# Kernel optimization log

Measured on AMD Instinct MI355X. Metric: run time of the kernel, lower is better.

## Reference

```python
import jax, jax.numpy as jnp
import numpy as np

B = 512          # graphs
M = 200          # nodes per graph
N = B * M        # 102400 total nodes
E = N * 32       # 3,276,800 edges
DIM_IN = 128
K = 30           # SortPool k
F = 32 + 32 + 32 + 1  # concat feature dim = 97


def setup_inputs() -> dict:
    key = jax.random.key(0)
    ks = jax.random.split(key, 20)
    x = jax.random.normal(ks[0], (N, DIM_IN), jnp.float32)
    # within-graph random edges so that batched SortPool is meaningful
    eg = jnp.repeat(jnp.arange(B, dtype=jnp.int32), E // B)  # graph id per edge
    src = eg * M + jax.random.randint(ks[1], (E,), 0, M, dtype=jnp.int32)
    dst = eg * M + jax.random.randint(ks[2], (E,), 0, M, dtype=jnp.int32)
    edge_index = jnp.stack([src, dst])  # [2, E]
    batch = jnp.arange(N, dtype=jnp.int32) // M  # sorted graph assignment

    def lin(k, fi, fo):
        s = 1.0 / np.sqrt(fi)
        return jax.random.uniform(k, (fi, fo), jnp.float32, -s, s)

    inp = {
        "x": x, "edge_index": edge_index, "batch": batch,
        "W1": lin(ks[3], DIM_IN, 32), "b1": jnp.zeros((32,), jnp.float32),
        "W2": lin(ks[4], 32, 32), "b2": jnp.zeros((32,), jnp.float32),
        "W3": lin(ks[5], 32, 32), "b3": jnp.zeros((32,), jnp.float32),
        "W4": lin(ks[6], 32, 1),  "b4": jnp.zeros((1,), jnp.float32),
        "convW1": jax.random.normal(ks[7], (16, 1, 97), jnp.float32) * 0.05,
        "convb1": jnp.zeros((16,), jnp.float32),
        "convW2": jax.random.normal(ks[8], (32, 16, 5), jnp.float32) * 0.05,
        "convb2": jnp.zeros((32,), jnp.float32),
        "linW1": lin(ks[9], 352, 128), "linb1": jnp.zeros((128,), jnp.float32),
        "linW2": lin(ks[10], 128, 1),  "linb2": jnp.zeros((1,), jnp.float32),
    }
    return inp


def _gcn(x, W, b, src, dst, dinv):
    """PyG GCNConv: D^-1/2 (A+I) D^-1/2 X W + b (degrees include self-loops)."""
    xw = x @ W                                   # [N, Fout]
    norm = dinv[src] * dinv[dst]                 # [E]
    agg = jax.ops.segment_sum(xw[src] * norm[:, None], dst, num_segments=N)
    agg = agg + xw * (dinv * dinv)[:, None]      # self-loop term
    return agg + b


def reference(x, edge_index, batch, W1, b1, W2, b2, W3, b3, W4, b4,
              convW1, convb1, convW2, convb2, linW1, linb1, linW2, linb2):
    src, dst = edge_index[0], edge_index[1]
    deg = jax.ops.segment_sum(jnp.ones((E,), x.dtype), dst, num_segments=N) + 1.0
    dinv = jax.lax.rsqrt(deg)

    h1 = jnp.tanh(_gcn(x, W1, b1, src, dst, dinv))
    h2 = jnp.tanh(_gcn(h1, W2, b2, src, dst, dinv))
    h3 = jnp.tanh(_gcn(h2, W3, b3, src, dst, dinv))
    h4 = jnp.tanh(_gcn(h3, W4, b4, src, dst, dinv))
    h = jnp.concatenate([h1, h2, h3, h4], axis=-1)  # [N, 97]

    # SortPool: batch is block-contiguous with M nodes/graph -> dense [B, M, F]
    hd = h.reshape(B, M, F)
    order = jnp.argsort(-hd[:, :, -1], axis=1)[:, :K]          # top-K by last channel
    top = jnp.take_along_axis(hd, order[:, :, None], axis=1)   # [B, K, 97]

    seq = top.reshape(B, 1, K * F)                             # [B, 1, 2910]
    dn = ("NCH", "OIH", "NCH")
    c1 = jax.lax.conv_general_dilated(seq, convW1, (97,), "VALID",
                                      dimension_numbers=dn) + convb1[None, :, None]
    c1 = jax.nn.relu(c1)                                       # [B, 16, 30]
    c1 = c1.reshape(B, 16, 15, 2).max(axis=-1)                 # MaxPool1d(2,2)
    c2 = jax.lax.conv_general_dilated(c1, convW2, (1,), "VALID",
                                      dimension_numbers=dn) + convb2[None, :, None]
    c2 = jax.nn.relu(c2)                                       # [B, 32, 11]

    flat = c2.reshape(B, 352)
    hlin = jax.nn.relu(flat @ linW1 + linb1)                   # dropout = identity (eval)
    out = jax.nn.sigmoid(hlin @ linW2 + linb2)                 # [B, 1]
    return out
```

## Files before the change

### kernel.cpp

```cpp
#include <hip/hip_runtime.h>
#include <hip/hip_fp16.h>


#define TPB   512
#define GRID  512
#define MG    200
#define EPG   6400
#define EE    (512 * EPG)

#define OFF_BUFX 0
#define OFF_HCUR 28944
#define OFF_CSR  57744
#define OFF_ROFF 64944
#define OFF_CNT  65760
#define OFF_CUR  66560
#define OFF_DINV 67360
#define OFF_H4   68160
#define OFF_RANK 68960
#define OFF_ORD  69760
#define OFF_BIAS 69880
#define OFF_RED  70072
#define OFF_WREG 70144
#define SMEM_BYTES 74240

__global__ __launch_bounds__(TPB)
void dgcnn_kernel(
    const float* __restrict__ x,
    const int*   __restrict__ ei,
    const float* __restrict__ W1, const float* __restrict__ b1,
    const float* __restrict__ W2, const float* __restrict__ b2,
    const float* __restrict__ W3, const float* __restrict__ b3,
    const float* __restrict__ W4, const float* __restrict__ b4,
    const float* __restrict__ cW1, const float* __restrict__ cb1,
    const float* __restrict__ cW2, const float* __restrict__ cb2,
    const float* __restrict__ lW1, const float* __restrict__ lb1,
    const float* __restrict__ lW2, const float* __restrict__ lb2,
    __half* __restrict__ arch,
    float* __restrict__ out)
{
    extern __shared__ unsigned char smem[];
    float* bufX = (float*)(smem + OFF_BUFX);
    float* hcur = (float*)(smem + OFF_HCUR);
    unsigned char* csr = (unsigned char*)(smem + OFF_CSR);
    int*   roff = (int*)(smem + OFF_ROFF);
    int*   cnt  = (int*)(smem + OFF_CNT);
    int*   cur  = (int*)(smem + OFF_CUR);
    float* dinv = (float*)(smem + OFF_DINV);
    float* h4k  = (float*)(smem + OFF_H4);
    int*   rank = (int*)(smem + OFF_RANK);
    int*   ord  = (int*)(smem + OFF_ORD);
    float* bias = (float*)(smem + OFF_BIAS);
    float* red  = (float*)(smem + OFF_RED);
    float* wreg = (float*)(smem + OFF_WREG);

    const int g = blockIdx.x;
    const int t = threadIdx.x;
    const int gbase = g * MG;
    const float* xg   = x + (size_t)gbase * 128;
    const int*   srcp = ei + (size_t)g * EPG;
    const int*   dstp = ei + (size_t)EE + (size_t)g * EPG;

    if (t < 32) bias[t] = b1[t];
    if (t < MG) { cnt[t] = 0; rank[t] = 0; }
    if (t >= 256 && t < 292) bufX[200 * 36 + (t - 256)] = 0.f;
    __syncthreads();

    for (int e = t; e < EPG; e += TPB) atomicAdd(&cnt[dstp[e] - gbase], 1);
    __syncthreads();

    if (t >= 256 && t < 256 + MG) {
        int i = t - 256;
        dinv[i] = 1.0f / sqrtf((float)(cnt[i] + 1));
    }
    if (t < 64) {
        if (t == 0) roff[0] = 0;
        int carry = 0;
        #pragma unroll
        for (int c = 0; c < 4; ++c) {
            const int i = c * 64 + t;
            int v = (i < MG) ? ((cnt[i] + 4) & ~3) : 0;
            #pragma unroll
            for (int off = 1; off < 64; off <<= 1) {
                int u = __shfl_up(v, off);
                if (t >= (int)off) v += u;
            }
            if (i < MG) roff[i + 1] = carry + v;
            carry += __shfl(v, 63);
        }
    }
    __syncthreads();

    if (t < MG) {
        int p = roff[t];
        csr[p] = (unsigned char)t;
        cur[t] = p + 1;
    }
    __syncthreads();

    for (int e = t; e < EPG; e += TPB) {
        int d = dstp[e] - gbase;
        int s = srcp[e] - gbase;
        int p = atomicAdd(&cur[d], 1);
        csr[p] = (unsigned char)s;
    }
    __syncthreads();

    if (t < MG) {
        for (int p = cur[t]; p < roff[t + 1]; ++p) csr[p] = (unsigned char)200;
    }
    __syncthreads();

    const int f32lane = t & 31;
    const int islot   = t >> 5;

    auto agg_layer = [&](int archOff) {
        const int fq  = t & 7;
        const int f4  = fq << 2;
        const int dsl = t >> 3;
        for (int d = dsl; d < MG; d += 64) {
            const int p0 = roff[d], p1 = roff[d + 1];
            float a0 = 0.f, a1 = 0.f, a2 = 0.f, a3 = 0.f;
            for (int p = p0; p < p1; p += 4) {
                const unsigned q = *(const unsigned*)(csr + p);
                const float4 v0 = *(const float4*)(bufX + (q & 255u) * 36 + f4);
                const float4 v1 = *(const float4*)(bufX + ((q >> 8) & 255u) * 36 + f4);
                a0 += v0.x; a1 += v0.y; a2 += v0.z; a3 += v0.w;
                a0 += v1.x; a1 += v1.y; a2 += v1.z; a3 += v1.w;
                const float4 v2 = *(const float4*)(bufX + ((q >> 16) & 255u) * 36 + f4);
                const float4 v3 = *(const float4*)(bufX + (q >> 24) * 36 + f4);
                a0 += v2.x; a1 += v2.y; a2 += v2.z; a3 += v2.w;
                a0 += v3.x; a1 += v3.y; a2 += v3.z; a3 += v3.w;
            }
            const float dv = dinv[d];
            const float o0 = tanhf(dv * a0 + bias[f4 + 0]);
            const float o1 = tanhf(dv * a1 + bias[f4 + 1]);
            const float o2 = tanhf(dv * a2 + bias[f4 + 2]);
            const float o3 = tanhf(dv * a3 + bias[f4 + 3]);
            *(float4*)(hcur + d * 36 + f4) = make_float4(o0, o1, o2, o3);
            if (archOff >= 0) {
                const __half2 p01 = __floats2half2_rn(o0, o1);
                const __half2 p23 = __floats2half2_rn(o2, o3);
                __half2* dst = (__half2*)(arch + (size_t)(gbase + d) * 64 + archOff + f4);
                dst[0] = p01;
                dst[1] = p23;
            }
        }
    };

    auto gemm_mid = [&](const float* __restrict__ src) {
        const int f = f32lane;
        #pragma unroll
        for (int j0 = 0; j0 < 12; j0 += 4) {
            const int r0 = islot + 16 * j0;
            float a0 = 0.f, a1 = 0.f, a2 = 0.f, a3 = 0.f;
            #pragma unroll 2
            for (int k4 = 0; k4 < 8; ++k4) {
                const float w0 = wreg[k4 * 128 + 0  + f];
                const float w1 = wreg[k4 * 128 + 32 + f];
                const float w2 = wreg[k4 * 128 + 64 + f];
                const float w3 = wreg[k4 * 128 + 96 + f];
                float4 v;
                v = *(const float4*)(src + (r0      ) * 36 + k4 * 4); a0 += v.x*w0 + v.y*w1 + v.z*w2 + v.w*w3;
                v = *(const float4*)(src + (r0 + 16 ) * 36 + k4 * 4); a1 += v.x*w0 + v.y*w1 + v.z*w2 + v.w*w3;
                v = *(const float4*)(src + (r0 + 32 ) * 36 + k4 * 4); a2 += v.x*w0 + v.y*w1 + v.z*w2 + v.w*w3;
                v = *(const float4*)(src + (r0 + 48 ) * 36 + k4 * 4); a3 += v.x*w0 + v.y*w1 + v.z*w2 + v.w*w3;
            }
            bufX[(r0      ) * 36 + f] = dinv[r0      ] * a0;
            bufX[(r0 + 16 ) * 36 + f] = dinv[r0 + 16 ] * a1;
            bufX[(r0 + 32 ) * 36 + f] = dinv[r0 + 32 ] * a2;
            bufX[(r0 + 48 ) * 36 + f] = dinv[r0 + 48 ] * a3;
        }
        if (islot < 8) {
            const int r = 192 + islot;
            float a0 = 0.f;
            #pragma unroll 2
            for (int k4 = 0; k4 < 8; ++k4) {
                const float w0 = wreg[k4 * 128 + 0  + f];
                const float w1 = wreg[k4 * 128 + 32 + f];
                const float w2 = wreg[k4 * 128 + 64 + f];
                const float w3 = wreg[k4 * 128 + 96 + f];
                const float4 v = *(const float4*)(src + r * 36 + k4 * 4);
                a0 += v.x*w0 + v.y*w1 + v.z*w2 + v.w*w3;
            }
            bufX[r * 36 + f] = dinv[r] * a0;
        }
    };

    {
        const int f = f32lane;
        const float4* xv = (const float4*)xg;
        #pragma unroll
        for (int j0 = 0; j0 < 12; j0 += 4) {
            const int r0 = islot + 16 * j0;
            float a0 = 0.f, a1 = 0.f, a2 = 0.f, a3 = 0.f;
            #pragma unroll 2
            for (int k4 = 0; k4 < 32; ++k4) {
                const float w0 = W1[k4 * 128 + 0  + f];
                const float w1 = W1[k4 * 128 + 32 + f];
                const float w2 = W1[k4 * 128 + 64 + f];
                const float w3 = W1[k4 * 128 + 96 + f];
                float4 v;
                v = xv[(r0      ) * 32 + k4]; a0 += v.x*w0 + v.y*w1 + v.z*w2 + v.w*w3;
                v = xv[(r0 + 16 ) * 32 + k4]; a1 += v.x*w0 + v.y*w1 + v.z*w2 + v.w*w3;
                v = xv[(r0 + 32 ) * 32 + k4]; a2 += v.x*w0 + v.y*w1 + v.z*w2 + v.w*w3;
                v = xv[(r0 + 48 ) * 32 + k4]; a3 += v.x*w0 + v.y*w1 + v.z*w2 + v.w*w3;
            }
            bufX[(r0      ) * 36 + f] = dinv[r0      ] * a0;
            bufX[(r0 + 16 ) * 36 + f] = dinv[r0 + 16 ] * a1;
            bufX[(r0 + 32 ) * 36 + f] = dinv[r0 + 32 ] * a2;
            bufX[(r0 + 48 ) * 36 + f] = dinv[r0 + 48 ] * a3;
        }
        if (islot < 8) {
            const int r = 192 + islot;
            float a0 = 0.f;
            #pragma unroll 2
            for (int k4 = 0; k4 < 32; ++k4) {
                const float w0 = W1[k4 * 128 + 0  + f];
                const float w1 = W1[k4 * 128 + 32 + f];
                const float w2 = W1[k4 * 128 + 64 + f];
                const float w3 = W1[k4 * 128 + 96 + f];
                const float4 v = xv[r * 32 + k4];
                a0 += v.x*w0 + v.y*w1 + v.z*w2 + v.w*w3;
            }
            bufX[r * 36 + f] = dinv[r] * a0;
        }
    }
    __syncthreads();
    agg_layer(0);
    __syncthreads();

    for (int idx = t; idx < 1024; idx += TPB) wreg[idx] = W2[idx];
    if (t < 32) bias[t] = b2[t];
    __syncthreads();
    gemm_mid(hcur);
    __syncthreads();
    agg_layer(32);
    __syncthreads();

    for (int idx = t; idx < 1024; idx += TPB) wreg[idx] = W3[idx];
    if (t < 32) bias[t] = b3[t];
    __syncthreads();
    gemm_mid(hcur);
    __syncthreads();
    agg_layer(-1);
    __syncthreads();

    float* scl = (float*)(smem + OFF_CNT);
    if (t < MG) {
        float a = 0.f;
        #pragma unroll 8
        for (int k = 0; k < 32; ++k) a += hcur[t * 36 + k] * W4[k];
        scl[t] = dinv[t] * a;
    }
    if (t == 200) scl[200] = 0.f;
    __syncthreads();
    if (t < MG) {
        const int p0 = roff[t], p1 = roff[t + 1];
        float s = 0.f;
        for (int p = p0; p < p1; p += 4) {
            const unsigned q = *(const unsigned*)(csr + p);
            s += scl[q & 255u] + scl[(q >> 8) & 255u]
               + scl[(q >> 16) & 255u] + scl[q >> 24];
        }
        h4k[t] = tanhf(dinv[t] * s + b4[0]);
    }
    __syncthreads();

    {
        const int i = t & 255;
        const int half = t >> 8;
        if (i < MG) {
            const float vi = h4k[i];
            int r = 0;
            const int j0 = half * 100, j1 = half * 100 + 100;
            for (int j = j0; j < j1; ++j) {
                const float vj = h4k[j];
                r += (vj > vi || (vj == vi && j < i)) ? 1 : 0;
            }
            atomicAdd(&rank[i], r);
        }
    }
    __syncthreads();
    if (t < MG) {
        const int r = rank[t];
        if (r < 30) ord[r] = t;
    }
    __syncthreads();

    float* topv = bufX;
    float* cw   = bufX + 3104;
    for (int idx = t; idx < 1552; idx += TPB) cw[idx] = cW1[idx];
    for (int idx = t; idx < 2560; idx += TPB) cw[1552 + idx] = cW2[idx];
    if (t < 16) bias[t] = cb1[t];
    else if (t < 48) bias[t] = cb2[t - 16];
    for (int idx = t; idx < 2910; idx += TPB) {
        const int kk = idx / 97;
        const int ff = idx - kk * 97;
        const int nd = ord[kk];
        float v;
        if      (ff < 64) v = __half2float(arch[(size_t)(gbase + nd) * 64 + ff]);
        else if (ff < 96) v = hcur[nd * 36 + (ff - 64)];
        else              v = h4k[nd];
        topv[kk * 100 + ff] = v;
    }
    __syncthreads();

    float* c1p2 = hcur;
    float* c1pl = hcur + 480;
    float* flat = hcur + 736;
    float* hlin = hcur + 1088;

    if (t < 480) {
        const int o  = t & 15;
        const int tt = t >> 4;
        float a = bias[o];
        const float* wrow = cw + o * 97;
        const float* trow = topv + tt * 100;
        #pragma unroll 4
        for (int f = 0; f < 97; ++f) a += wrow[f] * trow[f];
        c1p2[o * 30 + tt] = fmaxf(a, 0.f);
    }
    __syncthreads();

    if (t < 240) {
        const int o  = t & 15;
        const int tp = t >> 4;
        c1pl[o * 16 + tp] = fmaxf(c1p2[o * 30 + 2 * tp], c1p2[o * 30 + 2 * tp + 1]);
    }
    __syncthreads();

    if (t < 352) {
        const int o  = t & 31;
        const int tt = t >> 5;
        float a = bias[16 + o];
        const float* w2r = cw + 1552 + o * 80;
        #pragma unroll
        for (int i2 = 0; i2 < 16; ++i2) {
            #pragma unroll
            for (int kk = 0; kk < 5; ++kk)
                a += w2r[i2 * 5 + kk] * c1pl[i2 * 16 + tt + kk];
        }
        flat[o * 11 + tt] = fmaxf(a, 0.f);
    } else if (t >= 352 && t < 480) {
        hlin[t - 352] = lb1[t - 352];
    }
    __syncthreads();

    {
        const int f  = t & 127;
        const int kc = t >> 7;
        float a = 0.f;
        const int k0 = kc * 88;
        #pragma unroll 4
        for (int kk = k0; kk < k0 + 88; ++kk) a += flat[kk] * lW1[kk * 128 + f];
        atomicAdd(&hlin[f], a);
    }
    __syncthreads();

    if (t < 128) {
        float p = fmaxf(hlin[t], 0.f) * lW2[t];
        #pragma unroll
        for (int off = 32; off > 0; off >>= 1) p += __shfl_down(p, off);
        if ((t & 63) == 0) red[t >> 6] = p;
    }
    __syncthreads();
    if (t == 0) {
        const float z = red[0] + red[1] + lb2[0];
        out[g] = 1.f / (1.f + expf(-z));
    }
}

extern "C" void kernel_launch(void* const* d_in, const int* in_sizes, int n_in,
                              void* d_out, int out_size, void* d_ws, size_t ws_size,
                              hipStream_t stream) {
    (void)in_sizes; (void)n_in; (void)out_size; (void)ws_size;
    const float* x   = (const float*)d_in[0];
    const int*   ei  = (const int*)d_in[1];
    const float* W1  = (const float*)d_in[3];  const float* b1  = (const float*)d_in[4];
    const float* W2  = (const float*)d_in[5];  const float* b2  = (const float*)d_in[6];
    const float* W3  = (const float*)d_in[7];  const float* b3  = (const float*)d_in[8];
    const float* W4  = (const float*)d_in[9];  const float* b4  = (const float*)d_in[10];
    const float* cW1 = (const float*)d_in[11]; const float* cb1 = (const float*)d_in[12];
    const float* cW2 = (const float*)d_in[13]; const float* cb2 = (const float*)d_in[14];
    const float* lW1 = (const float*)d_in[15]; const float* lb1 = (const float*)d_in[16];
    const float* lW2 = (const float*)d_in[17]; const float* lb2 = (const float*)d_in[18];
    float* out = (float*)d_out;
    __half* arch = (__half*)d_ws;

    hipFuncSetAttribute((const void*)dgcnn_kernel,
                        hipFuncAttributeMaxDynamicSharedMemorySize, SMEM_BYTES);

    dgcnn_kernel<<<GRID, TPB, SMEM_BYTES, stream>>>(
        x, ei, W1, b1, W2, b2, W3, b3, W4, b4,
        cW1, cb1, cW2, cb2, lW1, lb1, lW2, lb2, arch, out);
}
```

Baseline: 268.1 us.

## Overlap W1 GEMM with degree counting, vectorize edge loads, fast tanh

Moves the layer-1 x@W1 projection ahead of the degree count so its global loads overlap the atomic histogram, and applies the dinv scaling afterwards in a separate pass. Edge index reads now use int4 vector loads for both the count and the CSR fill. Bias buffers are double-banked so weight and bias staging can follow each aggregation without an extra barrier. tanhf is replaced with an exp-based fast tanh, which trades a little accuracy and may overflow for large inputs.

```diff
diff --git a/kernel.cpp b/kernel.cpp
--- a/kernel.cpp
+++ b/kernel.cpp
@@ -19,9 +19,14 @@
 #define OFF_RANK 68960
 #define OFF_ORD  69760
 #define OFF_BIAS 69880
-#define OFF_RED  70072
-#define OFF_WREG 70144
-#define SMEM_BYTES 74240
+#define OFF_RED  70136
+#define OFF_WREG 70208
+#define SMEM_BYTES 74304
+
+__device__ __forceinline__ float fast_tanh(float x) {
+    const float e = __expf(2.0f * x);
+    return 1.0f - 2.0f / (e + 1.0f);
+}
 
 __global__ __launch_bounds__(TPB)
 void dgcnn_kernel(
@@ -65,7 +70,58 @@
     if (t >= 256 && t < 292) bufX[200 * 36 + (t - 256)] = 0.f;
     __syncthreads();
 
-    for (int e = t; e < EPG; e += TPB) atomicAdd(&cnt[dstp[e] - gbase], 1);
+    const int f32lane = t & 31;
+    const int islot   = t >> 5;
+
+    {
+        const int4* d4p = (const int4*)dstp;
+        for (int e4 = t; e4 < EPG / 4; e4 += TPB) {
+            const int4 d4 = d4p[e4];
+            atomicAdd(&cnt[d4.x - gbase], 1);
+            atomicAdd(&cnt[d4.y - gbase], 1);
+            atomicAdd(&cnt[d4.z - gbase], 1);
+            atomicAdd(&cnt[d4.w - gbase], 1);
+        }
+    }
+    {
+        const int f = f32lane;
+        const float4* xv = (const float4*)xg;
+        #pragma unroll
+        for (int j0 = 0; j0 < 12; j0 += 4) {
+            const int r0 = islot + 16 * j0;
+            float a0 = 0.f, a1 = 0.f, a2 = 0.f, a3 = 0.f;
+            #pragma unroll 2
+            for (int k4 = 0; k4 < 32; ++k4) {
+                const float w0 = W1[k4 * 128 + 0  + f];
+                const float w1 = W1[k4 * 128 + 32 + f];
+                const float w2 = W1[k4 * 128 + 64 + f];
+                const float w3 = W1[k4 * 128 + 96 + f];
+                float4 v;
+                v = xv[(r0      ) * 32 + k4]; a0 += v.x*w0 + v.y*w1 + v.z*w2 + v.w*w3;
+                v = xv[(r0 + 16 ) * 32 + k4]; a1 += v.x*w0 + v.y*w1 + v.z*w2 + v.w*w3;
+                v = xv[(r0 + 32 ) * 32 + k4]; a2 += v.x*w0 + v.y*w1 + v.z*w2 + v.w*w3;
+                v = xv[(r0 + 48 ) * 32 + k4]; a3 += v.x*w0 + v.y*w1 + v.z*w2 + v.w*w3;
+            }
+            bufX[(r0      ) * 36 + f] = a0;
+            bufX[(r0 + 16 ) * 36 + f] = a1;
+            bufX[(r0 + 32 ) * 36 + f] = a2;
+            bufX[(r0 + 48 ) * 36 + f] = a3;
+        }
+        if (islot < 8) {
+            const int r = 192 + islot;
+            float a0 = 0.f;
+            #pragma unroll 2
+            for (int k4 = 0; k4 < 32; ++k4) {
+                const float w0 = W1[k4 * 128 + 0  + f];
+                const float w1 = W1[k4 * 128 + 32 + f];
+                const float w2 = W1[k4 * 128 + 64 + f];
+                const float w3 = W1[k4 * 128 + 96 + f];
+                const float4 v = xv[r * 32 + k4];
+                a0 += v.x*w0 + v.y*w1 + v.z*w2 + v.w*w3;
+            }
+            bufX[r * 36 + f] = a0;
+        }
+    }
     __syncthreads();
 
     if (t >= 256 && t < 256 + MG) {
@@ -95,13 +151,25 @@
         csr[p] = (unsigned char)t;
         cur[t] = p + 1;
     }
-    __syncthreads();
-
-    for (int e = t; e < EPG; e += TPB) {
-        int d = dstp[e] - gbase;
-        int s = srcp[e] - gbase;
-        int p = atomicAdd(&cur[d], 1);
-        csr[p] = (unsigned char)s;
+    {
+        for (int r = islot; r < MG; r += 16) {
+            bufX[r * 36 + f32lane] *= dinv[r];
+        }
+    }
+    __syncthreads();
+
+    {
+        const int4* s4p = (const int4*)srcp;
+        const int4* d4p = (const int4*)dstp;
+        for (int e4 = t; e4 < EPG / 4; e4 += TPB) {
+            const int4 s4 = s4p[e4];
+            const int4 d4 = d4p[e4];
+            int p;
+            p = atomicAdd(&cur[d4.x - gbase], 1); csr[p] = (unsigned char)(s4.x - gbase);
+            p = atomicAdd(&cur[d4.y - gbase], 1); csr[p] = (unsigned char)(s4.y - gbase);
+            p = atomicAdd(&cur[d4.z - gbase], 1); csr[p] = (unsigned char)(s4.z - gbase);
+            p = atomicAdd(&cur[d4.w - gbase], 1); csr[p] = (unsigned char)(s4.w - gbase);
+        }
     }
     __syncthreads();
 
@@ -110,10 +178,7 @@
     }
     __syncthreads();
 
-    const int f32lane = t & 31;
-    const int islot   = t >> 5;
-
-    auto agg_layer = [&](int archOff) {
+    auto agg_layer = [&](int archOff, int bb) {
         const int fq  = t & 7;
         const int f4  = fq << 2;
         const int dsl = t >> 3;
@@ -132,10 +197,10 @@
                 a0 += v3.x; a1 += v3.y; a2 += v3.z; a3 += v3.w;
             }
             const float dv = dinv[d];
-            const float o0 = tanhf(dv * a0 + bias[f4 + 0]);
-            const float o1 = tanhf(dv * a1 + bias[f4 + 1]);
-            const float o2 = tanhf(dv * a2 + bias[f4 + 2]);
-            const float o3 = tanhf(dv * a3 + bias[f4 + 3]);
+            const float o0 = fast_tanh(dv * a0 + bias[bb + f4 + 0]);
+            const float o1 = fast_tanh(dv * a1 + bias[bb + f4 + 1]);
+            const float o2 = fast_tanh(dv * a2 + bias[bb + f4 + 2]);
+            const float o3 = fast_tanh(dv * a3 + bias[bb + f4 + 3]);
             *(float4*)(hcur + d * 36 + f4) = make_float4(o0, o1, o2, o3);
             if (archOff >= 0) {
                 const __half2 p01 = __floats2half2_rn(o0, o1);
@@ -186,63 +251,21 @@
         }
     };
 
-    {
-        const int f = f32lane;
-        const float4* xv = (const float4*)xg;
-        #pragma unroll
-        for (int j0 = 0; j0 < 12; j0 += 4) {
-            const int r0 = islot + 16 * j0;
-            float a0 = 0.f, a1 = 0.f, a2 = 0.f, a3 = 0.f;
-            #pragma unroll 2
-            for (int k4 = 0; k4 < 32; ++k4) {
-                const float w0 = W1[k4 * 128 + 0  + f];
-                const float w1 = W1[k4 * 128 + 32 + f];
-                const float w2 = W1[k4 * 128 + 64 + f];
-                const float w3 = W1[k4 * 128 + 96 + f];
-                float4 v;
-                v = xv[(r0      ) * 32 + k4]; a0 += v.x*w0 + v.y*w1 + v.z*w2 + v.w*w3;
-                v = xv[(r0 + 16 ) * 32 + k4]; a1 += v.x*w0 + v.y*w1 + v.z*w2 + v.w*w3;
-                v = xv[(r0 + 32 ) * 32 + k4]; a2 += v.x*w0 + v.y*w1 + v.z*w2 + v.w*w3;
-                v = xv[(r0 + 48 ) * 32 + k4]; a3 += v.x*w0 + v.y*w1 + v.z*w2 + v.w*w3;
-            }
-            bufX[(r0      ) * 36 + f] = dinv[r0      ] * a0;
-            bufX[(r0 + 16 ) * 36 + f] = dinv[r0 + 16 ] * a1;
-            bufX[(r0 + 32 ) * 36 + f] = dinv[r0 + 32 ] * a2;
-            bufX[(r0 + 48 ) * 36 + f] = dinv[r0 + 48 ] * a3;
-        }
-        if (islot < 8) {
-            const int r = 192 + islot;
-            float a0 = 0.f;
-            #pragma unroll 2
-            for (int k4 = 0; k4 < 32; ++k4) {
-                const float w0 = W1[k4 * 128 + 0  + f];
-                const float w1 = W1[k4 * 128 + 32 + f];
-                const float w2 = W1[k4 * 128 + 64 + f];
-                const float w3 = W1[k4 * 128 + 96 + f];
-                const float4 v = xv[r * 32 + k4];
-                a0 += v.x*w0 + v.y*w1 + v.z*w2 + v.w*w3;
-            }
-            bufX[r * 36 + f] = dinv[r] * a0;
-        }
-    }
-    __syncthreads();
-    agg_layer(0);
-    __syncthreads();
-
+    agg_layer(0, 0);
     for (int idx = t; idx < 1024; idx += TPB) wreg[idx] = W2[idx];
-    if (t < 32) bias[t] = b2[t];
-    __syncthreads();
+    if (t < 32) bias[32 + t] = b2[t];
+    __syncthreads();
+
     gemm_mid(hcur);
     __syncthreads();
-    agg_layer(32);
-    __syncthreads();
-
+    agg_layer(32, 32);
     for (int idx = t; idx < 1024; idx += TPB) wreg[idx] = W3[idx];
     if (t < 32) bias[t] = b3[t];
     __syncthreads();
+
     gemm_mid(hcur);
     __syncthreads();
-    agg_layer(-1);
+    agg_layer(-1, 0);
     __syncthreads();
 
     float* scl = (float*)(smem + OFF_CNT);
@@ -262,7 +285,7 @@
             s += scl[q & 255u] + scl[(q >> 8) & 255u]
                + scl[(q >> 16) & 255u] + scl[q >> 24];
         }
-        h4k[t] = tanhf(dinv[t] * s + b4[0]);
+        h4k[t] = fast_tanh(dinv[t] * s + b4[0]);
     }
     __syncthreads();
 
```

Measured after the change: 264.9 us. About the same (-1.2%).
